# Kernel optimization log

Measured on AMD Instinct MI355X. Metric: run time of the kernel, lower is better.

The kernel has to match this reference:

```python
import jax, jax.numpy as jnp
import numpy as np

E = 256
CH = 16  # channel rows; features viewed as (16,16)


def _sigmoid_np(x):
    return 1.0 / (1.0 + np.exp(-x))


def _schedule(emb, comp_l, comp_r, cb, seqs):
    """Phase 1 (host/numpy, mirrors the detached torch control flow):
    runs the iterative argmax-merge tree construction and records the
    integer merge schedule (new composed node pairs per iteration) and the
    (target, ctx_left, ctx_right) prediction triples. Matches Banyan.compose."""
    emb = np.asarray(emb, np.float32)
    sl = _sigmoid_np(np.asarray(comp_l, np.float32))
    sr = _sigmoid_np(np.asarray(comp_r, np.float32))
    cbn = np.asarray(cb, np.float32)
    seqs = np.asarray(seqs, np.int64)

    uniq = np.unique(seqs)
    lookup = np.zeros(uniq.max() + 1, np.int64)
    lookup[uniq] = np.arange(len(uniq))
    lookup[uniq[-1]] = -1  # max unique value acts as pad sentinel (lookup[-1] = -1)
    index = lookup[seqs].copy()
    tokens = uniq[:-1]

    nodes = emb[tokens]  # detached node features used only for similarity / schedule

    def comp(f):  # f: (K,2,16,16)
        return (f[:, 0] * sl + f[:, 1] * sr + cbn).reshape(f.shape[0], -1)

    pair_src = np.zeros((0, 2), np.int64)
    pair_dst = np.zeros((0,), np.int64)
    new_pairs, targets = [], []
    B, W = index.shape

    while W != 1:
        valid = index != -1
        f = nodes[np.clip(index, 0, None)]              # (B,W,E)
        a, b = f[:, :-1], f[:, 1:]
        na = np.linalg.norm(a, axis=-1)
        nb = np.linalg.norm(b, axis=-1)
        cos = (a * b).sum(-1) / np.maximum(na * nb, 1e-8)
        cos = np.where(valid[:, 1:], cos, -np.inf)       # right slot padded -> -inf
        ms_all = np.argmax(cos, axis=1)
        active = ~np.all(index[:, 1:] == -1, axis=1)
        rows = np.nonzero(active)[0]
        ms = ms_all[rows]
        lp, rp = ms, ms + 1
        src = np.stack([index[rows, lp], index[rows, rp]], 1)  # (A,2)

        # dedup against existing composed pairs, then unique new pairs (sorted)
        if pair_src.shape[0] > 0 and src.shape[0] > 0:
            exists = (src[:, None, :] == pair_src[None]).all(-1).any(1)
            newp = src[~exists]
        else:
            newp = src
        if newp.shape[0] > 0:
            newp = np.unique(newp, axis=0)
        base = nodes.shape[0]
        if newp.shape[0] > 0:
            nodes = np.concatenate([nodes, comp(nodes[newp].reshape(-1, 2, CH, CH))], 0)
            pair_src = np.concatenate([pair_src, newp], 0)
            pair_dst = np.concatenate([pair_dst, base + np.arange(newp.shape[0])], 0)
        new_pairs.append(newp.astype(np.int64))

        # neighbourhood targets (get_neighbours): l_t block then r_t block
        lefts, rights = src[:, 0], src[:, 1]
        ls = index[rows, lp - 1].copy()
        ls[lp - 1 == -1] = -1
        rs = index[rows, np.minimum(rp + 1, W - 1)].copy()
        rs[rp + 1 == W] = -2
        targets.append(np.stack([lefts, ls, rights], 1))
        targets.append(np.stack([rights, lefts, rs], 1))

        # point both merged slots at the (possibly shared) composed node id
        if src.shape[0] > 0:
            eq = (src[:, None, :] == pair_src[None]).all(-1)
            nid = pair_dst[eq.argmax(1)]
            index[rows, lp] = nid
            index[rows, rp] = nid

        # reduce frontier: active rows drop the left merge slot, inactive drop last col
        keep = np.ones_like(index, dtype=bool)
        keep[rows, ms] = False
        keep[~active, -1] = False
        index = index[keep].reshape(B, W - 1)
        W -= 1

    targets = np.concatenate(targets, 0).astype(np.int64)
    return tokens, new_pairs, targets


def _replay(emb, comp_l, comp_r, cb, sos, eos, tokens, new_pairs, targets):
    """Phase 2 (jax, differentiable): rebuild node features following the
    recorded schedule, then compute the context->target cross entropy."""
    sl = jax.nn.sigmoid(comp_l)
    sr = jax.nn.sigmoid(comp_r)
    feats = emb[tokens]                                    # (n_tok, E)
    for p in new_pairs:
        if p.shape[0] == 0:
            continue
        f = feats[p].reshape(-1, 2, CH, CH)                # (K,2,16,16)
        feats = jnp.concatenate([feats, (f[:, 0] * sl + f[:, 1] * sr + cb).reshape(-1, E)], 0)
    feats = jnp.concatenate([feats, eos[None, :], sos[None, :]], 0)
    N = feats.shape[0]
    t = np.where(targets < 0, targets + N, targets)        # wrap -1 -> sos, -2 -> eos
    l = feats[t[:, 1]].reshape(-1, CH, CH)
    r = feats[t[:, 2]].reshape(-1, CH, CH)
    outs = (l * sl + r * sr + cb).reshape(-1, E)           # (T,E)
    logits = outs @ feats.T                                # (T,N)
    logp = jax.nn.log_softmax(logits, axis=-1)
    return -jnp.mean(logp[jnp.arange(t.shape[0]), t[:, 0]])


def setup_inputs() -> dict:
    key = jax.random.key(0)
    k1, k2, k3, k4, k5, k6, k7 = jax.random.split(key, 7)
    V, B, L = 30000, 64, 64
    tok = jax.random.randint(k1, (B, L), 0, V - 1, dtype=jnp.int32)
    lengths = jax.random.randint(k2, (B,), L // 2, L + 1, dtype=jnp.int32)
    lengths = lengths.at[0].set(L // 2)  # guarantee pad token (V-1) is present
    x = jnp.where(jnp.arange(L)[None, :] < lengths[:, None], tok, V - 1)
    return {
        "x": x,
        "emb": jax.random.normal(k3, (V, E), jnp.float32),
        "comp_l": jax.random.uniform(k4, (CH,), jnp.float32, 0.6, 0.9),
        "comp_r": jax.random.uniform(k5, (CH,), jnp.float32, 0.6, 0.9),
        "cb": jnp.zeros((CH,), jnp.float32),
        "sos": 0.02 * jax.random.normal(k6, (E,), jnp.float32),
        "eos": 0.02 * jax.random.normal(k7, (E,), jnp.float32),
    }


def reference(x, emb, comp_l, comp_r, cb, sos, eos):
    tokens, new_pairs, targets = _schedule(emb, comp_l, comp_r, cb, x)
    return _replay(emb, comp_l, comp_r, cb, sos, eos, tokens, new_pairs, targets)
```

## Files before the change

### kernel.cpp

```cpp
#include <hip/hip_runtime.h>
#include <math.h>


#define NMAX 8192
#define PRES 30720
#define HBITS 13
#define HSIZE 8192
#define HMASK 8191
#define LOG2E 1.44269504f
#define LN2 0.69314718f
#define NSLAB 8

typedef float f32x4 __attribute__((ext_vector_type(4)));
typedef short short8 __attribute__((ext_vector_type(8)));

__device__ __forceinline__ unsigned hash0(int key) {
    return (((unsigned)key) * 2654435761u) >> (32 - HBITS);
}

__device__ __forceinline__ unsigned short f2bf(float f) {
    unsigned u = __float_as_uint(f);
    unsigned r = ((u >> 16) & 1u) + 0x7FFFu;
    return (unsigned short)((u + r) >> 16);
}

__device__ __forceinline__ float rdl_f(float v, int lane) {
    return __int_as_float(__builtin_amdgcn_readlane(__float_as_int(v), lane));
}

#define SUM_STEP(CTRL, X) \
    X += __int_as_float(__builtin_amdgcn_update_dpp(0, __float_as_int(X), CTRL, 0xF, 0xF, true));
#define SUM3_REDUCE(A, B, C) {                                                  \
    SUM_STEP(0x121, A) SUM_STEP(0x121, B) SUM_STEP(0x121, C)                    \
    SUM_STEP(0x122, A) SUM_STEP(0x122, B) SUM_STEP(0x122, C)                    \
    SUM_STEP(0x124, A) SUM_STEP(0x124, B) SUM_STEP(0x124, C)                    \
    SUM_STEP(0x128, A) SUM_STEP(0x128, B) SUM_STEP(0x128, C)                    \
    A = rdl_f(A, 0) + rdl_f(A, 16) + rdl_f(A, 32) + rdl_f(A, 48);               \
    B = rdl_f(B, 0) + rdl_f(B, 16) + rdl_f(B, 32) + rdl_f(B, 48);               \
    C = rdl_f(C, 0) + rdl_f(C, 16) + rdl_f(C, 32) + rdl_f(C, 48);               \
}
#define ARGMAX_STEP(CTRL, V, I) {                                               \
    float _ov = __int_as_float(__builtin_amdgcn_update_dpp(0, __float_as_int(V), CTRL, 0xF, 0xF, true)); \
    int _oi = __builtin_amdgcn_update_dpp(0, I, CTRL, 0xF, 0xF, true);          \
    if (_ov > V || (_ov == V && _oi < I)) { V = _ov; I = _oi; }                 \
}
#define ARGMAX_REDUCE(V, I) {                                                   \
    ARGMAX_STEP(0x121, V, I) ARGMAX_STEP(0x122, V, I)                           \
    ARGMAX_STEP(0x124, V, I) ARGMAX_STEP(0x128, V, I)                           \
    float _v0 = rdl_f(V, 0), _v1 = rdl_f(V, 16), _v2 = rdl_f(V, 32), _v3 = rdl_f(V, 48); \
    int _i0 = __builtin_amdgcn_readlane(I, 0), _i1 = __builtin_amdgcn_readlane(I, 16);   \
    int _i2 = __builtin_amdgcn_readlane(I, 32), _i3 = __builtin_amdgcn_readlane(I, 48);  \
    V = _v0; I = _i0;                                                           \
    if (_v1 > V || (_v1 == V && _i1 < I)) { V = _v1; I = _i1; }                 \
    if (_v2 > V || (_v2 == V && _i2 < I)) { V = _v2; I = _i2; }                 \
    if (_v3 > V || (_v3 == V && _i3 < I)) { V = _v3; I = _i3; }                 \
}

__global__ __launch_bounds__(1024) void prep_kernel(
    const int* __restrict__ x, int* __restrict__ tokens,
    int* __restrict__ meta, int* __restrict__ index_g) {
    __shared__ int pres[PRES];
    __shared__ int part[1024];
    int tid = threadIdx.x;
    for (int i = tid; i < PRES; i += 1024) pres[i] = 0;
    __syncthreads();
    for (int i = tid; i < 4096; i += 1024) pres[x[i]] = 1;
    __syncthreads();
    int base = tid * 30;
    int loc[30];
    int s = 0;
#pragma unroll
    for (int i = 0; i < 30; ++i) { loc[i] = s; s += pres[base + i]; }
    part[tid] = s;
    __syncthreads();
    for (int off = 1; off < 1024; off <<= 1) {
        int v = (tid >= off) ? part[tid - off] : 0;
        __syncthreads();
        part[tid] += v;
        __syncthreads();
    }
    int excl = (tid == 0) ? 0 : part[tid - 1];
    int total = part[1023];
#pragma unroll
    for (int i = 0; i < 30; ++i) {
        if (pres[base + i]) tokens[excl + loc[i]] = base + i;
    }
    if (tid == 0) { meta[0] = total; meta[1] = total - 1; }
    __syncthreads();
#pragma unroll
    for (int i = 0; i < 30; ++i) pres[base + i] = excl + loc[i];
    __syncthreads();
    for (int i = tid; i < 4096; i += 1024) {
        int r = pres[x[i]];
        index_g[i] = (r == total - 1) ? -1 : r;
    }
}

__global__ __launch_bounds__(64) void prefeats_kernel(
    const float* __restrict__ emb, const int* __restrict__ tokens,
    const int* __restrict__ meta, const int* __restrict__ index_g,
    float* __restrict__ feats, float* __restrict__ norms,
    float* __restrict__ cos_g) {
    int g = blockIdx.x;
    int k = threadIdx.x;
    if (g < 4096) {
        int n = g;
        if (n >= meta[1]) return;
        int t = tokens[n];
        float4 v = ((const float4*)(emb + (size_t)t * 256))[k];
        ((float4*)(feats + (size_t)n * 256))[k] = v;
        float ss = v.x * v.x + v.y * v.y + v.z * v.z + v.w * v.w;
#pragma unroll
        for (int off = 32; off >= 1; off >>= 1) ss += __shfl_down(ss, off);
        if (k == 0) norms[n] = sqrtf(ss);
        return;
    }
    int idx = g - 4096;
    int b = idx / 63, j = idx % 63;
    int l = index_g[b * 64 + j], r = index_g[b * 64 + j + 1];
    float c = -INFINITY;
    if (r != -1) {
        int tl = tokens[l], tr = tokens[r];
        float4 a = ((const float4*)(emb + (size_t)tl * 256))[k];
        float4 bb = ((const float4*)(emb + (size_t)tr * 256))[k];
        float d = a.x * bb.x + a.y * bb.y + a.z * bb.z + a.w * bb.w;
        float na = a.x * a.x + a.y * a.y + a.z * a.z + a.w * a.w;
        float nb = bb.x * bb.x + bb.y * bb.y + bb.z * bb.z + bb.w * bb.w;
#pragma unroll
        for (int off = 32; off >= 1; off >>= 1) {
            d += __shfl_down(d, off);
            na += __shfl_down(na, off);
            nb += __shfl_down(nb, off);
        }
        c = d / fmaxf(sqrtf(na) * sqrtf(nb), 1e-8f);
    }
    if (k == 0) cos_g[b * 64 + j] = c;
}


__global__ __launch_bounds__(64) void treebuild_kernel(
    const float* __restrict__ feats, const float* __restrict__ norms_g,
    const int* __restrict__ index_g, const float* __restrict__ cos_g,
    float* __restrict__ rowfeats, int4* __restrict__ rec,
    const float* __restrict__ comp_l, const float* __restrict__ comp_r,
    const float* __restrict__ cb) {
    __shared__ float lf[127][256];
    __shared__ int4 s_rec[63];
    int b = blockIdx.x;
    int lane = threadIdx.x;
    int c0 = 4 * (lane & 3);
    float4 sl4 = make_float4(1.f / (1.f + __expf(-comp_l[c0])),
                             1.f / (1.f + __expf(-comp_l[c0 + 1])),
                             1.f / (1.f + __expf(-comp_l[c0 + 2])),
                             1.f / (1.f + __expf(-comp_l[c0 + 3])));
    float4 sr4 = make_float4(1.f / (1.f + __expf(-comp_r[c0])),
                             1.f / (1.f + __expf(-comp_r[c0 + 1])),
                             1.f / (1.f + __expf(-comp_r[c0 + 2])),
                             1.f / (1.f + __expf(-comp_r[c0 + 3])));
    float4 cb4 = make_float4(cb[c0], cb[c0 + 1], cb[c0 + 2], cb[c0 + 3]);

    int gid = index_g[b * 64 + lane];
    int isreal = (gid >= 0) ? 1 : 0;
    for (int j = 0; j < 64; ++j) {
        int g = index_g[b * 64 + j];
        int gc = g < 0 ? 0 : g;
        ((float4*)&lf[j][0])[lane] = ((const float4*)(feats + (size_t)gc * 256))[lane];
    }
    float n0 = (gid >= 0) ? norms_g[gid] : 0.f;
    float n1 = 0.f;
    float cosr = (lane < 63) ? cos_g[b * 64 + lane] : -INFINITY;
    int locid = lane;
    unsigned long long alive = ~0ull;
    int nreal = 64 - __popcll(__ballot(gid < 0));

    float Mv = cosr; int Mi = lane;
    ARGMAX_REDUCE(Mv, Mi);

    for (int it = 0; it < 63; ++it) {
        int act = (nreal >= 2) ? 1 : 0;
        int p = Mi;
        unsigned long long after = (alive >> 1) >> p;
        int q = (p + 1 + __builtin_ctzll(after | 0x8000000000000000ull)) & 63;
        unsigned long long bel = alive & ((1ull << p) - 1ull);
        int pp = bel ? (63 - __builtin_clzll(bel)) : -1;
        unsigned long long aft2 = (q < 63) ? (alive >> (q + 1)) : 0ull;
        int ssp = aft2 ? (q + 1 + __builtin_ctzll(aft2)) : -1;
        int l_loc = __builtin_amdgcn_readlane(locid, p);
        int r_loc = __builtin_amdgcn_readlane(locid, q);
        int lsl = __builtin_amdgcn_readlane(locid, pp < 0 ? 0 : pp);
        int rsl = __builtin_amdgcn_readlane(locid, ssp < 0 ? 0 : ssp);
        int ls_loc = (pp >= 0) ? lsl : -1;
        int rs_loc = (ssp >= 0) ? rsl : -2;
        int Creal = (ssp >= 0) ? __builtin_amdgcn_readlane(isreal, ssp) : 0;
        if (lane == 0)
            s_rec[it] = make_int4(act ? l_loc : -9, r_loc, ls_loc, rs_loc);
        if (act) {
            float4 a = ((const float4*)&lf[l_loc][0])[lane];
            float4 bb = ((const float4*)&lf[r_loc][0])[lane];
            float4 av = (pp >= 0) ? ((const float4*)&lf[ls_loc < 0 ? 0 : ls_loc][0])[lane]
                                  : make_float4(0.f, 0.f, 0.f, 0.f);
            float4 cv = Creal ? ((const float4*)&lf[rs_loc < 0 ? 0 : rs_loc][0])[lane]
                              : make_float4(0.f, 0.f, 0.f, 0.f);
            float mv = (lane == p || lane == q || lane == pp) ? -INFINITY : cosr;
            float Mv2 = mv; int Mi2 = lane;
            ARGMAX_REDUCE(Mv2, Mi2);
            int nl = 64 + it;
            float4 v;
            v.x = a.x * sl4.x + bb.x * sr4.x + cb4.x;
            v.y = a.y * sl4.y + bb.y * sr4.y + cb4.y;
            v.z = a.z * sl4.z + bb.z * sr4.z + cb4.z;
            v.w = a.w * sl4.w + bb.w * sr4.w + cb4.w;
            ((float4*)&lf[nl][0])[lane] = v;
            float sv = v.x * v.x + v.y * v.y + v.z * v.z + v.w * v.w;
            float da = av.x * v.x + av.y * v.y + av.z * v.z + av.w * v.w;
            float dc = cv.x * v.x + cv.y * v.y + cv.z * v.z + cv.w * v.w;
            SUM3_REDUCE(sv, da, dc);
            float nn = sqrtf(sv);
            if (lane == it) n1 = nn;
            float nA = 1.f, nC = 1.f;
            if (pp >= 0) nA = (ls_loc < 64) ? rdl_f(n0, ls_loc) : rdl_f(n1, ls_loc - 64);
            if (Creal)   nC = (rs_loc < 64) ? rdl_f(n0, rs_loc) : rdl_f(n1, rs_loc - 64);
            float cosA = da * __builtin_amdgcn_rcpf(fmaxf(nA * nn, 1e-8f));
            float cosC = Creal ? (dc * __builtin_amdgcn_rcpf(fmaxf(nn * nC, 1e-8f))) : -INFINITY;
            if (lane == p) { cosr = cosC; locid = nl; }
            if (lane == pp) cosr = cosA;
            if (lane == q) cosr = -INFINITY;
            if (pp >= 0 && (cosA > Mv2 || (cosA == Mv2 && pp < Mi2))) { Mv2 = cosA; Mi2 = pp; }
            if (cosC > Mv2 || (cosC == Mv2 && p < Mi2)) { Mv2 = cosC; Mi2 = p; }
            Mv = Mv2; Mi = Mi2;
            alive &= ~(1ull << q);
            nreal -= 1;
        }
    }
    for (int it = 0; it < 63; ++it) {
        ((float4*)(rowfeats + ((size_t)b * 63 + it) * 256))[lane] =
            ((const float4*)&lf[64 + it][0])[lane];
    }
    if (lane < 63) rec[b * 63 + lane] = s_rec[lane];
}


__global__ __launch_bounds__(64) void idassign_kernel(
    const int4* __restrict__ rec, const int* __restrict__ index_g,
    int* __restrict__ targets, int* __restrict__ meta, int* __restrict__ newsrc) {
    __shared__ int s_map[64][128];
    __shared__ int s_hk[HSIZE], s_hv[HSIZE];
    int b = threadIdx.x;
    for (int i = b; i < HSIZE; i += 64) s_hk[i] = -1;
    for (int i = b; i < 4096; i += 64) s_map[i >> 6][i & 63] = index_g[i];
    int N0 = meta[1];
    int Ncur = N0, Tcur = 0;
    __syncthreads();
    int4 R = rec[b * 63];
    for (int it = 0; it < 63; ++it) {
        int4 Rn = R;
        if (it + 1 < 63) Rn = rec[b * 63 + it + 1];
        int act = (R.x != -9) ? 1 : 0;
        int l_g = 0, r_g = 0, key = 0, nid = 0;
        int ls_g = -1, rs_g = -2;
        unsigned h = 0;
        int won = 0, need = 0;
        if (act) {
            l_g = s_map[b][R.x];
            r_g = s_map[b][R.y];
            ls_g = (R.z >= 0) ? s_map[b][R.z] : R.z;
            rs_g = (R.w >= 0) ? s_map[b][R.w] : R.w;
            key = (l_g << HBITS) | r_g;
            h = hash0(key);
            need = 1;
        }
        while (__any(need)) {
            if (need) {
                int prev = atomicCAS(&s_hk[h], -1, key);
                if (prev == -1) { won = 1; need = 0; }
                else if (prev == key) { need = 0; }
                else { h = (h + 1) & HMASK; }
            }
        }
        unsigned long long actmask = __ballot(act != 0);
        unsigned long long winmask = __ballot(won != 0);
        unsigned long long below = (1ull << b) - 1ull;
        int ar = __popcll(actmask & below);
        int nact = __popcll(actmask);
        int newc = __popcll(winmask);
        if (won) {
            nid = Ncur + __popcll(winmask & below);
            s_hv[h] = nid;
        }
        __syncthreads();
        if (act && !won) nid = s_hv[h];
        if (won) newsrc[nid - N0] = (b << 6) | it;
        if (act) {
            int o1 = Tcur + ar;
            targets[o1 * 3 + 0] = l_g;
            targets[o1 * 3 + 1] = ls_g;
            targets[o1 * 3 + 2] = r_g;
            int o2 = Tcur + nact + ar;
            targets[o2 * 3 + 0] = r_g;
            targets[o2 * 3 + 1] = l_g;
            targets[o2 * 3 + 2] = rs_g;
            s_map[b][64 + it] = nid;
        }
        Ncur += newc;
        Tcur += 2 * nact;
        R = Rn;
    }
    if (b == 0) { meta[2] = Ncur; meta[3] = Tcur; meta[4] = Ncur - N0; }
}


__global__ __launch_bounds__(64) void materialize_kernel(
    const float* __restrict__ rowfeats, const int* __restrict__ newsrc,
    const int* __restrict__ meta, float* __restrict__ feats,
    const float* __restrict__ eos, const float* __restrict__ sos) {
    int g = blockIdx.x;
    int lane = threadIdx.x;
    if (g == 4032) {
        int n = meta[2];
        ((float4*)(feats + (size_t)n * 256))[lane] = ((const float4*)eos)[lane];
        ((float4*)(feats + (size_t)(n + 1) * 256))[lane] = ((const float4*)sos)[lane];
        return;
    }
    if (g >= meta[4]) return;
    int pk = newsrc[g];
    int b = pk >> 6, it = pk & 63;
    int N0 = meta[1];
    ((float4*)(feats + (size_t)(N0 + g) * 256))[lane] =
        ((const float4*)(rowfeats + ((size_t)b * 63 + it) * 256))[lane];
}

__global__ __launch_bounds__(256) void convout_kernel(
    const float* __restrict__ feats, const int* __restrict__ targets,
    const int* __restrict__ meta, const float* __restrict__ comp_l,
    const float* __restrict__ comp_r, const float* __restrict__ cb,
    short8* __restrict__ fhT, unsigned short* __restrict__ oh,
    float* __restrict__ tdot) {
    if (blockIdx.x < 1024) {
        int g = blockIdx.x * 256 + threadIdx.x;
        int tile = g >> 9, rem = g & 511;
        int ks = rem >> 6, lane64 = rem & 63;
        int kq = lane64 >> 4, col = lane64 & 15;
        int row = tile * 16 + col;
        int e0 = (ks * 4 + kq) * 8;
        const float4* src = (const float4*)(feats + (size_t)row * 256 + e0);
        float4 v0 = src[0], v1 = src[1];
        short8 o;
        o[0] = (short)f2bf(v0.x); o[1] = (short)f2bf(v0.y);
        o[2] = (short)f2bf(v0.z); o[3] = (short)f2bf(v0.w);
        o[4] = (short)f2bf(v1.x); o[5] = (short)f2bf(v1.y);
        o[6] = (short)f2bf(v1.z); o[7] = (short)f2bf(v1.w);
        fhT[g] = o;
        return;
    }
    int T = meta[3];
    int Ntot = meta[2] + 2;
    int t = (blockIdx.x - 1024) * 4 + (threadIdx.x >> 6);
    if (t >= T) return;
    int lane = threadIdx.x & 63;
    int c0 = 4 * (lane & 3);
    float4 sl4 = make_float4(1.f / (1.f + __expf(-comp_l[c0])),
                             1.f / (1.f + __expf(-comp_l[c0 + 1])),
                             1.f / (1.f + __expf(-comp_l[c0 + 2])),
                             1.f / (1.f + __expf(-comp_l[c0 + 3])));
    float4 sr4 = make_float4(1.f / (1.f + __expf(-comp_r[c0])),
                             1.f / (1.f + __expf(-comp_r[c0 + 1])),
                             1.f / (1.f + __expf(-comp_r[c0 + 2])),
                             1.f / (1.f + __expf(-comp_r[c0 + 3])));
    float4 cb4 = make_float4(cb[c0], cb[c0 + 1], cb[c0 + 2], cb[c0 + 3]);
    int t0 = targets[t * 3 + 0];
    int i1 = targets[t * 3 + 1], i2 = targets[t * 3 + 2];
    if (i1 < 0) i1 += Ntot;
    if (i2 < 0) i2 += Ntot;
    float4 a = ((const float4*)(feats + (size_t)i1 * 256))[lane];
    float4 b = ((const float4*)(feats + (size_t)i2 * 256))[lane];
    float4 ft = ((const float4*)(feats + (size_t)t0 * 256))[lane];
    float4 v;
    v.x = a.x * sl4.x + b.x * sr4.x + cb4.x;
    v.y = a.y * sl4.y + b.y * sr4.y + cb4.y;
    v.z = a.z * sl4.z + b.z * sr4.z + cb4.z;
    v.w = a.w * sl4.w + b.w * sr4.w + cb4.w;
    float d = v.x * ft.x + v.y * ft.y + v.z * ft.z + v.w * ft.w;
#pragma unroll
    for (int off = 32; off >= 1; off >>= 1) d += __shfl_down(d, off);
    if (lane == 0) tdot[t] = d;
    ushort4 h;
    h.x = f2bf(v.x * LOG2E); h.y = f2bf(v.y * LOG2E);
    h.z = f2bf(v.z * LOG2E); h.w = f2bf(v.w * LOG2E);
    ((ushort4*)(oh + (size_t)t * 256))[lane] = h;
}

__global__ __launch_bounds__(512) void loss_mfma_kernel(
    const short8* __restrict__ fhT, const unsigned short* __restrict__ oh,
    const int* __restrict__ meta, float2* __restrict__ partial) {
    __shared__ short8 lds_b[1024];
    __shared__ float s_m[64][2], s_s[64][2];
    int T = meta[3];
    int Ntot = meta[2] + 2;
    int row0 = blockIdx.x * 64;
    if (row0 >= T) return;
    int slab = blockIdx.y;
    int P = (Ntot + 32 * NSLAB - 1) / (32 * NSLAB);
    int cstart = slab * (P << 5);
    int cend = min(Ntot, cstart + (P << 5));
    int tid = threadIdx.x, lane = tid & 63, w = tid >> 6;
    int mq = w >> 1, nq = w & 1;
    int mrow = row0 + mq * 16 + (lane & 15);
    int kq = lane >> 4;
    const short8* pah = (const short8*)(oh + (size_t)mrow * 256);
    short8 Ah[8];
#pragma unroll
    for (int ks = 0; ks < 8; ++ks) Ah[ks] = pah[ks * 4 + kq];
    float m0 = -1e30f, m1 = -1e30f, m2 = -1e30f, m3 = -1e30f;
    float s0 = 0.f, s1 = 0.f, s2 = 0.f, s3 = 0.f;
    if (cstart < cend) {
        const short8* sp = fhT + ((size_t)(cstart >> 4)) * 512;
        lds_b[tid] = sp[tid];
        lds_b[tid + 512] = sp[tid + 512];
        __syncthreads();
    }
    for (int nb = cstart; nb < cend; nb += 32) {
        short8 g0, g1;
        bool more = (nb + 32) < cend;
        if (more) {
            const short8* sn = fhT + ((size_t)((nb + 32) >> 4)) * 512;
            g0 = sn[tid];
            g1 = sn[tid + 512];
        }
        const short8* pb = lds_b + nq * 512;
        f32x4 a0 = {0.f, 0.f, 0.f, 0.f}, a1 = a0;
#pragma unroll
        for (int ks = 0; ks < 4; ++ks) {
            a0 = __builtin_amdgcn_mfma_f32_16x16x32_bf16(Ah[ks], pb[ks * 64 + lane], a0, 0, 0, 0);
            a1 = __builtin_amdgcn_mfma_f32_16x16x32_bf16(Ah[ks + 4], pb[(ks + 4) * 64 + lane], a1, 0, 0, 0);
        }
        int col = nb + nq * 16 + (lane & 15);
        bool cv = col < cend;
        float v0 = cv ? (a0[0] + a1[0]) : -INFINITY;
        float v1 = cv ? (a0[1] + a1[1]) : -INFINITY;
        float v2 = cv ? (a0[2] + a1[2]) : -INFINITY;
        float v3 = cv ? (a0[3] + a1[3]) : -INFINITY;
        float d0 = v0 - m0, d1 = v1 - m1, d2 = v2 - m2, d3 = v3 - m3;
        if (d0 > 32.f) { s0 = s0 * exp2f(-d0) + 1.f; m0 = v0; } else s0 += exp2f(d0);
        if (d1 > 32.f) { s1 = s1 * exp2f(-d1) + 1.f; m1 = v1; } else s1 += exp2f(d1);
        if (d2 > 32.f) { s2 = s2 * exp2f(-d2) + 1.f; m2 = v2; } else s2 += exp2f(d2);
        if (d3 > 32.f) { s3 = s3 * exp2f(-d3) + 1.f; m3 = v3; } else s3 += exp2f(d3);
        if (more) {
            __syncthreads();
            lds_b[tid] = g0;
            lds_b[tid + 512] = g1;
            __syncthreads();
        }
    }
#pragma unroll
    for (int off = 1; off < 16; off <<= 1) {
        float mo, so, mn;
        mo = __shfl_xor(m0, off); so = __shfl_xor(s0, off);
        mn = fmaxf(m0, mo); s0 = s0 * exp2f(m0 - mn) + so * exp2f(mo - mn); m0 = mn;
        mo = __shfl_xor(m1, off); so = __shfl_xor(s1, off);
        mn = fmaxf(m1, mo); s1 = s1 * exp2f(m1 - mn) + so * exp2f(mo - mn); m1 = mn;
        mo = __shfl_xor(m2, off); so = __shfl_xor(s2, off);
        mn = fmaxf(m2, mo); s2 = s2 * exp2f(m2 - mn) + so * exp2f(mo - mn); m2 = mn;
        mo = __shfl_xor(m3, off); so = __shfl_xor(s3, off);
        mn = fmaxf(m3, mo); s3 = s3 * exp2f(m3 - mn) + so * exp2f(mo - mn); m3 = mn;
    }
    if ((lane & 15) == 0) {
        int rbase = mq * 16 + kq * 4;
        s_m[rbase + 0][nq] = m0; s_s[rbase + 0][nq] = s0;
        s_m[rbase + 1][nq] = m1; s_s[rbase + 1][nq] = s1;
        s_m[rbase + 2][nq] = m2; s_s[rbase + 2][nq] = s2;
        s_m[rbase + 3][nq] = m3; s_s[rbase + 3][nq] = s3;
    }
    __syncthreads();
    if (tid < 64) {
        float ma = s_m[tid][0], mb = s_m[tid][1];
        float mn = fmaxf(ma, mb);
        float ss = s_s[tid][0] * exp2f(ma - mn) + s_s[tid][1] * exp2f(mb - mn);
        partial[(size_t)slab * NMAX + row0 + tid] = make_float2(mn, ss);
    }
}

__global__ __launch_bounds__(1024) void combine_kernel(
    const float2* __restrict__ partial, const float* __restrict__ tdot,
    const int* __restrict__ meta, float* __restrict__ out) {
    __shared__ float red[16];
    int T = meta[3];
    float loss = 0.f;
    for (int r = threadIdx.x; r < T; r += 1024) {
        float2 ps[NSLAB];
        float mn = -1e30f;
#pragma unroll
        for (int s = 0; s < NSLAB; ++s) {
            ps[s] = partial[(size_t)s * NMAX + r];
            mn = fmaxf(mn, ps[s].x);
        }
        float ss = 0.f;
#pragma unroll
        for (int s = 0; s < NSLAB; ++s) ss += ps[s].y * exp2f(ps[s].x - mn);
        loss += (mn + __log2f(ss)) * LN2 - tdot[r];
    }
#pragma unroll
    for (int off = 32; off >= 1; off >>= 1) loss += __shfl_down(loss, off);
    if ((threadIdx.x & 63) == 0) red[threadIdx.x >> 6] = loss;
    __syncthreads();
    if (threadIdx.x < 16) {
        loss = red[threadIdx.x];
#pragma unroll
        for (int off = 8; off >= 1; off >>= 1) loss += __shfl_down(loss, off);
        if (threadIdx.x == 0) out[0] = loss / (float)T;
    }
}

extern "C" void kernel_launch(void* const* d_in, const int* in_sizes, int n_in,
                              void* d_out, int out_size, void* d_ws, size_t ws_size,
                              hipStream_t stream) {
    const int* x = (const int*)d_in[0];
    const float* emb = (const float*)d_in[1];
    const float* comp_l = (const float*)d_in[2];
    const float* comp_r = (const float*)d_in[3];
    const float* cb = (const float*)d_in[4];
    const float* sos = (const float*)d_in[5];
    const float* eos = (const float*)d_in[6];
    float* out = (float*)d_out;

    float* feats = (float*)d_ws;
    float* norms = feats + (size_t)NMAX * 256;
    int* index_g = (int*)(norms + NMAX);
    float* cos_g = (float*)(index_g + 4096);
    int* tokens = (int*)(cos_g + 4096);
    int* targets = tokens + 4096;
    int* meta = targets + NMAX * 3;
    float* tdot = (float*)(meta + 64);
    float2* partial = (float2*)(tdot + NMAX);
    int4* rec = (int4*)(partial + NSLAB * NMAX);
    int* newsrc = (int*)(rec + 64 * 63);
    float* rowfeats = (float*)(newsrc + 4096);
    short8* fhT = (short8*)(rowfeats + (size_t)64 * 63 * 256);
    unsigned short* oh = (unsigned short*)(fhT + (size_t)NMAX * 32);

    prep_kernel<<<1, 1024, 0, stream>>>(x, tokens, meta, index_g);
    prefeats_kernel<<<8128, 64, 0, stream>>>(emb, tokens, meta, index_g,
                                             feats, norms, cos_g);
    treebuild_kernel<<<64, 64, 0, stream>>>(feats, norms, index_g, cos_g,
                                            rowfeats, rec, comp_l, comp_r, cb);
    idassign_kernel<<<1, 64, 0, stream>>>(rec, index_g, targets, meta, newsrc);
    materialize_kernel<<<4033, 64, 0, stream>>>(rowfeats, newsrc, meta, feats, eos, sos);
    convout_kernel<<<3040, 256, 0, stream>>>(feats, targets, meta, comp_l, comp_r,
                                             cb, fhT, oh, tdot);
    loss_mfma_kernel<<<dim3(126, NSLAB), 512, 0, stream>>>(fhT, oh, meta, partial);
    combine_kernel<<<1, 1024, 0, stream>>>(partial, tdot, meta, out);
}
```

Before: 200.4 us.

## Double-buffer LDS tiles in loss kernel and use wave-shuffle scan in prep

```diff
diff --git a/kernel.cpp b/kernel.cpp
--- a/kernel.cpp
+++ b/kernel.cpp
@@ -61,32 +61,46 @@
     int* __restrict__ meta, int* __restrict__ index_g) {
     __shared__ int pres[PRES];
     __shared__ int part[1024];
+    __shared__ int wsum[16];
     int tid = threadIdx.x;
+    int lane = tid & 63, wave = tid >> 6;
     for (int i = tid; i < PRES; i += 1024) pres[i] = 0;
     __syncthreads();
     for (int i = tid; i < 4096; i += 1024) pres[x[i]] = 1;
     __syncthreads();
     int base = tid * 30;
     int loc[30];
-    int s = 0;
-#pragma unroll
-    for (int i = 0; i < 30; ++i) { loc[i] = s; s += pres[base + i]; }
-    part[tid] = s;
-    __syncthreads();
-    for (int off = 1; off < 1024; off <<= 1) {
-        int v = (tid >= off) ? part[tid - off] : 0;
-        __syncthreads();
-        part[tid] += v;
-        __syncthreads();
-    }
-    int excl = (tid == 0) ? 0 : part[tid - 1];
-    int total = part[1023];
+    int tot = 0;
+#pragma unroll
+    for (int i = 0; i < 30; ++i) { loc[i] = tot; tot += pres[base + i]; }
+    int sc = tot;
+#pragma unroll
+    for (int off = 1; off < 64; off <<= 1) {
+        int v = __shfl_up(sc, off);
+        if (lane >= off) sc += v;
+    }
+    if (lane == 63) wsum[wave] = sc;
+    __syncthreads();
+    if (tid < 16) {
+        int wv = wsum[tid];
+#pragma unroll
+        for (int off = 1; off < 16; off <<= 1) {
+            int v = __shfl_up(wv, off);
+            if (tid >= off) wv += v;
+        }
+        wsum[tid] = wv;
+    }
+    __syncthreads();
+    int incl = sc + ((wave == 0) ? 0 : wsum[wave - 1]);
+    int excl = incl - tot;
+    part[tid] = incl;
 #pragma unroll
     for (int i = 0; i < 30; ++i) {
         if (pres[base + i]) tokens[excl + loc[i]] = base + i;
     }
+    __syncthreads();
+    int total = part[1023];
     if (tid == 0) { meta[0] = total; meta[1] = total - 1; }
-    __syncthreads();
 #pragma unroll
     for (int i = 0; i < 30; ++i) pres[base + i] = excl + loc[i];
     __syncthreads();
@@ -392,7 +406,7 @@
 __global__ __launch_bounds__(512) void loss_mfma_kernel(
     const short8* __restrict__ fhT, const unsigned short* __restrict__ oh,
     const int* __restrict__ meta, float2* __restrict__ partial) {
-    __shared__ short8 lds_b[1024];
+    __shared__ short8 lds_b[2][1024];
     __shared__ float s_m[64][2], s_s[64][2];
     int T = meta[3];
     int Ntot = meta[2] + 2;
@@ -412,10 +426,11 @@
     for (int ks = 0; ks < 8; ++ks) Ah[ks] = pah[ks * 4 + kq];
     float m0 = -1e30f, m1 = -1e30f, m2 = -1e30f, m3 = -1e30f;
     float s0 = 0.f, s1 = 0.f, s2 = 0.f, s3 = 0.f;
+    int cur = 0;
     if (cstart < cend) {
         const short8* sp = fhT + ((size_t)(cstart >> 4)) * 512;
-        lds_b[tid] = sp[tid];
-        lds_b[tid + 512] = sp[tid + 512];
+        lds_b[0][tid] = sp[tid];
+        lds_b[0][tid + 512] = sp[tid + 512];
         __syncthreads();
     }
     for (int nb = cstart; nb < cend; nb += 32) {
@@ -426,7 +441,7 @@
             g0 = sn[tid];
             g1 = sn[tid + 512];
         }
-        const short8* pb = lds_b + nq * 512;
+        const short8* pb = &lds_b[cur][nq * 512];
         f32x4 a0 = {0.f, 0.f, 0.f, 0.f}, a1 = a0;
 #pragma unroll
         for (int ks = 0; ks < 4; ++ks) {
@@ -445,10 +460,10 @@
         if (d2 > 32.f) { s2 = s2 * exp2f(-d2) + 1.f; m2 = v2; } else s2 += exp2f(d2);
         if (d3 > 32.f) { s3 = s3 * exp2f(-d3) + 1.f; m3 = v3; } else s3 += exp2f(d3);
         if (more) {
+            lds_b[cur ^ 1][tid] = g0;
+            lds_b[cur ^ 1][tid + 512] = g1;
             __syncthreads();
-            lds_b[tid] = g0;
-            lds_b[tid + 512] = g1;
-            __syncthreads();
+            cur ^= 1;
         }
     }
 #pragma unroll
```

After: 197.7 us (median of 2 runs). Within noise of the previous version (-1.4%).
